# Kernel optimization log

Hardware: AMD Instinct MI355X
Metric: run time of the kernel (lower is better)

The kernel has to match this reference:

```python
import jax, jax.numpy as jnp
import numpy as np

ROPE_THETA = 10000.0

def apply_rope(x, positions):
    # x: [b, h, s, d], positions: [s]
    d = x.shape[-1]
    inv_freq = ROPE_THETA ** (-jnp.arange(0, d, 2, dtype=jnp.float32) / d)  # [d/2]
    ang = positions.astype(jnp.float32)[:, None] * inv_freq[None, :]        # [s, d/2]
    cos = jnp.cos(ang)
    sin = jnp.sin(ang)
    x1 = x[..., 0::2]
    x2 = x[..., 1::2]
    r1 = x1 * cos - x2 * sin
    r2 = x1 * sin + x2 * cos
    # interleave back to [..., d]
    return jnp.stack([r1, r2], axis=-1).reshape(x.shape)

def setup_inputs() -> dict:
    key = jax.random.key(0)
    k1, k2, k3 = jax.random.split(key, 3)
    b, s, d_model = 4, 2048, 1024
    x = jax.random.normal(k1, (b, s, d_model), dtype=jnp.float32)
    wqkv = jax.random.normal(k2, (3 * d_model, d_model), dtype=jnp.float32) * (d_model ** -0.5)
    wo = jax.random.normal(k3, (d_model, d_model), dtype=jnp.float32) * (d_model ** -0.5)
    token_positions = jnp.arange(s, dtype=jnp.int64 if jax.config.jax_enable_x64 else jnp.int32)
    return {"x": x, "wqkv": wqkv, "wo": wo, "token_positions": token_positions}

def reference(x, wqkv, wo, token_positions):
    b, s, d_model = x.shape
    num_heads = 16
    d_head = d_model // num_heads
    # fused QKV projection (Linear: y = x @ W.T)
    qkv = jnp.einsum('bse,fe->bsf', x, wqkv)  # [b, s, 3*d_model]
    q, k, v = jnp.split(qkv, 3, axis=-1)
    def to_heads(t):
        return t.reshape(b, s, num_heads, d_head).transpose(0, 2, 1, 3)  # [b, h, s, d]
    q, k, v = to_heads(q), to_heads(k), to_heads(v)
    q = apply_rope(q, token_positions)
    k = apply_rope(k, token_positions)
    scores = jnp.einsum('bhqd,bhkd->bhqk', q, k) / jnp.sqrt(jnp.asarray(d_head, dtype=x.dtype))
    causal = jnp.tril(jnp.ones((s, s), dtype=bool))  # [s, s]
    scores = jnp.where(causal, scores, -jnp.inf)
    weights = jax.nn.softmax(scores, axis=-1)
    y = jnp.einsum('bhqk,bhkd->bhqd', weights, v)
    y = y.transpose(0, 2, 1, 3).reshape(b, s, d_model)
    return jnp.einsum('bse,fe->bsf', y, wo)
```

## Files before the change

### kernel.cpp

```cpp
#include <hip/hip_runtime.h>
#include <stdint.h>


typedef __attribute__((ext_vector_type(8))) short bf16x8;
typedef __attribute__((ext_vector_type(4))) float f32x4;
typedef __attribute__((ext_vector_type(8))) unsigned short u16x8;
typedef __attribute__((ext_vector_type(4))) unsigned short u16x4;
typedef __attribute__((ext_vector_type(4))) unsigned int u32x4;

#define NB 4
#define NS 2048
#define NH 16
#define DH 64
#define DM 1024
#define BH (NB*NH)

static __device__ __forceinline__ unsigned short f2bf(float f){
  unsigned u = __builtin_bit_cast(unsigned, f);
  u += 0x7fffu + ((u >> 16) & 1u);
  return (unsigned short)(u >> 16);
}
static __device__ __forceinline__ float bf2f(unsigned short h){
  unsigned u = ((unsigned)h) << 16;
  return __builtin_bit_cast(float, u);
}
static __device__ __forceinline__ unsigned cvt_pk_bf16(float lo, float hi){
  unsigned r;
  asm("v_cvt_pk_bf16_f32 %0, %1, %2" : "=v"(r) : "v"(lo), "v"(hi));
  return r;
}
static __device__ __forceinline__ f32x4 mfma16(bf16x8 a, bf16x8 b, f32x4 c){
  return __builtin_amdgcn_mfma_f32_16x16x32_bf16(a, b, c, 0, 0, 0);
}
static __device__ __forceinline__ void gld_lds16(const void* g, void* l){
  __builtin_amdgcn_global_load_lds((const __attribute__((address_space(1))) unsigned int*)g,
                                   (__attribute__((address_space(3))) unsigned int*)l,
                                   16, 0, 0);
}

__global__ __launch_bounds__(256) void cvt_all(const float* __restrict__ x,
                                               const float* __restrict__ wqkv,
                                               const float* __restrict__ wo,
                                               const int* __restrict__ pos,
                                               unsigned short* __restrict__ xb,
                                               unsigned short* __restrict__ wqkvb,
                                               unsigned short* __restrict__ wob,
                                               float* __restrict__ ct,
                                               float* __restrict__ st){
  int stride = gridDim.x * blockDim.x;
  for (int i = blockIdx.x * blockDim.x + threadIdx.x; i < 3211264; i += stride){
    if (i < 3145728){
      const float* src; unsigned short* dst; int j;
      if (i < 2097152){ src = x; dst = xb; j = i; }
      else if (i < 2883584){ src = wqkv; dst = wqkvb; j = i - 2097152; }
      else { src = wo; dst = wob; j = i - 2883584; }
      f32x4 v = *(const f32x4*)(src + (size_t)j * 4);
      u16x4 o;
      o[0] = f2bf(v[0]); o[1] = f2bf(v[1]); o[2] = f2bf(v[2]); o[3] = f2bf(v[3]);
      *(u16x4*)(dst + (size_t)j * 4) = o;
    } else {
      int t = i - 3145728;
      int s = t >> 5, fi = t & 31;
      float p = (float)pos[s];
      float freq = exp2f(-(float)(2 * fi) * (13.287712379549449f / 64.f));
      float a = p * freq;
      ct[t] = cosf(a);
      st[t] = sinf(a);
    }
  }
}

__global__ __launch_bounds__(256) void rope_qk(unsigned short* __restrict__ buf,
                                               const float* __restrict__ ct,
                                               const float* __restrict__ st){
  size_t t  = (size_t)blockIdx.x * 256 + threadIdx.x;
  size_t e0 = t * 8;
  int dh0 = (int)(e0 & 63);
  int s   = (int)((e0 >> 6) & (NS - 1));
  u16x8 v = *(const u16x8*)(buf + e0);
  f32x4 c  = *(const f32x4*)(ct + s * 32 + (dh0 >> 1));
  f32x4 sn = *(const f32x4*)(st + s * 32 + (dh0 >> 1));
  u16x8 o;
#pragma unroll
  for (int i = 0; i < 4; i++){
    float x1 = bf2f(v[2*i]), x2 = bf2f(v[2*i+1]);
    o[2*i]   = f2bf(x1 * c[i] - x2 * sn[i]);
    o[2*i+1] = f2bf(x1 * sn[i] + x2 * c[i]);
  }
  *(u16x8*)(buf + e0) = o;
}

template<int BM, int BN, int MF, int NFR, int EPI, int RING, int OCC>
__global__ __launch_bounds__((BM/(MF*16))*(BN/(NFR*16))*64, OCC)
void gemm_ring(const unsigned short* __restrict__ A,
               const unsigned short* __restrict__ Bm,
               void* __restrict__ out0, void* __restrict__ out1,
               void* __restrict__ out2, int M, int N, int K){
  constexpr int WM = BM / (MF * 16);
  constexpr int WN = BN / (NFR * 16);
  constexpr int T  = WM * WN * 64;
  constexpr int LA = BM * 4 / T;
  constexpr int LB = BN * 4 / T;
  constexpr int L  = LA + LB;
  __shared__ __attribute__((aligned(16))) unsigned short As[RING][BM * 32];
  __shared__ __attribute__((aligned(16))) unsigned short Bs[RING][BN * 32];
  int tid = threadIdx.x;
  int w = tid >> 6, l = tid & 63;
  int lr = l & 15, lk = l >> 4;
  int m0 = blockIdx.y * BM, n0 = blockIdx.x * BN;
  int wr = (w / WN) * (MF * 16), wc = (w % WN) * (NFR * 16);

  const int nt = K >> 5;

  auto stage = [&](int t, int buf){
    int k0 = t * 32;
#pragma unroll
    for (int i = 0; i < LA; i++){
      int f = i * T + tid;
      int row = f >> 2, c = f & 3;
      int gc = (c ^ ((row >> 1) & 3)) * 8;
      gld_lds16(A + (size_t)(m0 + row) * K + k0 + gc, &As[buf][(i * T + w * 64) * 8]);
    }
#pragma unroll
    for (int i = 0; i < LB; i++){
      int f = i * T + tid;
      int row = f >> 2, c = f & 3;
      int gc = (c ^ ((row >> 1) & 3)) * 8;
      gld_lds16(Bm + (size_t)(n0 + row) * K + k0 + gc, &Bs[buf][(i * T + w * 64) * 8]);
    }
  };

  f32x4 zero = {0.f, 0.f, 0.f, 0.f};
  f32x4 acc[MF][NFR];
#pragma unroll
  for (int a = 0; a < MF; a++)
#pragma unroll
    for (int b = 0; b < NFR; b++) acc[a][b] = zero;

#pragma unroll
  for (int p = 0; p < RING - 1; p++) stage(p, p);
  asm volatile("s_waitcnt vmcnt(%0)" :: "i"((RING - 2) * L) : "memory");
  __builtin_amdgcn_sched_barrier(0);
  __builtin_amdgcn_s_barrier();
  __builtin_amdgcn_sched_barrier(0);

  int buf = 0;
  for (int t = 0; t < nt; ++t){
    bf16x8 af[MF], bfr[NFR];
#pragma unroll
    for (int mf = 0; mf < MF; mf++){
      int row = wr + mf * 16 + lr;
      af[mf] = *(const bf16x8*)&As[buf][row * 32 + ((lk ^ ((row >> 1) & 3)) * 8)];
    }
#pragma unroll
    for (int nf = 0; nf < NFR; nf++){
      int row = wc + nf * 16 + lr;
      bfr[nf] = *(const bf16x8*)&Bs[buf][row * 32 + ((lk ^ ((row >> 1) & 3)) * 8)];
    }
    if (t + RING - 1 < nt){
      int sb = buf - 1; if (sb < 0) sb = RING - 1;
      stage(t + RING - 1, sb);
    }
    __builtin_amdgcn_s_setprio(1);
#pragma unroll
    for (int mf = 0; mf < MF; mf++)
#pragma unroll
      for (int nf = 0; nf < NFR; nf++)
        acc[mf][nf] = mfma16(af[mf], bfr[nf], acc[mf][nf]);
    __builtin_amdgcn_s_setprio(0);
    if (RING >= 4){
      if (t + 3 < nt)      { asm volatile("s_waitcnt vmcnt(%0)" :: "i"(2 * L) : "memory"); }
      else if (t + 2 < nt) { asm volatile("s_waitcnt vmcnt(%0)" :: "i"(L) : "memory"); }
      else if (t + 1 < nt) { asm volatile("s_waitcnt vmcnt(0)" ::: "memory"); }
    } else {
      if (t + 2 < nt)      { asm volatile("s_waitcnt vmcnt(%0)" :: "i"(L) : "memory"); }
      else if (t + 1 < nt) { asm volatile("s_waitcnt vmcnt(0)" ::: "memory"); }
    }
    __builtin_amdgcn_sched_barrier(0);
    __builtin_amdgcn_s_barrier();
    __builtin_amdgcn_sched_barrier(0);
    buf = buf + 1; if (buf == RING) buf = 0;
  }

  if (EPI == 0){
    unsigned short* q  = (unsigned short*)out0;
    unsigned short* k  = (unsigned short*)out1;
    unsigned short* vt = (unsigned short*)out2;
#pragma unroll
    for (int mf = 0; mf < MF; mf++)
#pragma unroll
      for (int nf = 0; nf < NFR; nf++)
#pragma unroll
        for (int j = 0; j < 4; j++){
          int m = m0 + wr + mf * 16 + lk * 4 + j;
          int n = n0 + wc + nf * 16 + lr;
          int part = n >> 10, c = n & 1023;
          int h = c >> 6, dh = c & 63;
          int b = m >> 11, s = m & (NS - 1);
          unsigned short val = f2bf(acc[mf][nf][j]);
          if (part == 2){
            vt[((size_t)((b * NH + h) * DH + dh)) * NS + s] = val;
          } else {
            size_t off = ((size_t)(b * NH + h) * NS + s) * DH + dh;
            ((part == 0) ? q : k)[off] = val;
          }
        }
  } else {
    float* C = (float*)out0;
#pragma unroll
    for (int mf = 0; mf < MF; mf++)
#pragma unroll
      for (int nf = 0; nf < NFR; nf++)
#pragma unroll
        for (int j = 0; j < 4; j++){
          int m = m0 + wr + mf * 16 + lk * 4 + j;
          int n = n0 + wc + nf * 16 + lr;
          C[(size_t)m * N + n] = acc[mf][nf][j];
        }
  }
}

__global__ __launch_bounds__(256, 3) void fa_kernel(const unsigned short* __restrict__ qb_,
                                                    const unsigned short* __restrict__ kbuf,
                                                    const unsigned short* __restrict__ vtb,
                                                    unsigned short* __restrict__ yb,
                                                    const float* __restrict__ ct_,
                                                    const float* __restrict__ st_){
  __shared__ __attribute__((aligned(16))) unsigned short Kl[2][4096];
  __shared__ __attribute__((aligned(16))) unsigned short Vl[2][4096];
  __shared__ __attribute__((aligned(16))) unsigned short Pl[4][32 * 76];
  int tid = threadIdx.x;
  int w = tid >> 6, l = tid & 63;
  int lr = l & 15, lk = l >> 4;
  int qb = 15 - blockIdx.y;
  int bh = blockIdx.x;
  int b = bh >> 4, h = bh & 15;
  int qr0 = qb * 128 + w * 32;
  const unsigned short* Q  = qb_  + (size_t)bh * NS * DH;
  const unsigned short* Kp = kbuf + (size_t)bh * NS * DH;
  const unsigned short* VT = vtb  + (size_t)bh * DH * NS;
  unsigned short* Pw = &Pl[w][0];

  int r8  = l >> 3;
  int swc = ((l & 7) ^ (r8 & 7)) * 8;

  auto stage = [&](int buf, int t){
    int kbase = t * 64;
    if (w < 2){
#pragma unroll
      for (int ii = 0; ii < 4; ii++){
        int i = w * 4 + ii;
        gld_lds16(Kp + (size_t)(kbase + i * 8 + r8) * DH + swc, &Kl[buf][i * 512]);
      }
    } else {
#pragma unroll
      for (int ii = 0; ii < 4; ii++){
        int i = (w - 2) * 4 + ii;
        gld_lds16(VT + (size_t)(i * 8 + r8) * NS + kbase + swc, &Vl[buf][i * 512]);
      }
    }
  };

  const float SC = 0.18033688011112042f;
  bf16x8 qf[2][2];
#pragma unroll
  for (int mf = 0; mf < 2; mf++){
    int srow = qr0 + mf * 16 + lr;
    const unsigned short* qrow = Q + (size_t)srow * DH;
    const float* ctr = ct_ + srow * 32;
    const float* str = st_ + srow * 32;
#pragma unroll
    for (int ks = 0; ks < 2; ks++){
      u16x8 raw = *(const u16x8*)(qrow + ks * 32 + lk * 8);
      f32x4 cc = *(const f32x4*)(ctr + ks * 16 + lk * 4);
      f32x4 ss = *(const f32x4*)(str + ks * 16 + lk * 4);
      u32x4 wds;
#pragma unroll
      for (int p = 0; p < 4; p++){
        float c2 = cc[p] * SC, s2 = ss[p] * SC;
        float x1 = bf2f(raw[2*p]), x2 = bf2f(raw[2*p+1]);
        wds[p] = cvt_pk_bf16(x1 * c2 - x2 * s2, x1 * s2 + x2 * c2);
      }
      qf[mf][ks] = __builtin_bit_cast(bf16x8, wds);
    }
  }

  f32x4 zero = {0.f, 0.f, 0.f, 0.f};
  f32x4 O[2][4];
  float lsum[2];
#pragma unroll
  for (int mf = 0; mf < 2; mf++){
#pragma unroll
    for (int nf = 0; nf < 4; nf++) O[mf][nf] = zero;
    lsum[mf] = 0.f;
  }

  const int ntile = 2 * qb + 2;

  stage(0, 0);
  __syncthreads();

  int cur = 0;
  for (int t = 0; t < ntile; ++t){
    int kbase = t * 64;
    if (t + 1 < ntile) stage(cur ^ 1, t + 1);

    if (kbase <= qr0 + 31){
      bf16x8 kf[4][2];
#pragma unroll
      for (int nf = 0; nf < 4; nf++){
        int row = nf * 16 + lr;
        int ro = row * 64, sw = (row & 7) << 3;
#pragma unroll
        for (int ks = 0; ks < 2; ks++)
          kf[nf][ks] = *(const bf16x8*)&Kl[cur][ro + ((ks * 32 + lk * 8) ^ sw)];
      }
      bf16x8 vf[2][4];
#pragma unroll
      for (int nfd = 0; nfd < 4; nfd++){
        int row = nfd * 16 + lr;
        int ro = row * 64, sw = (row & 7) << 3;
#pragma unroll
        for (int ks = 0; ks < 2; ks++)
          vf[ks][nfd] = *(const bf16x8*)&Vl[cur][ro + ((ks * 32 + lk * 8) ^ sw)];
      }

      f32x4 sa[2][4];
#pragma unroll
      for (int mf = 0; mf < 2; mf++)
#pragma unroll
        for (int nf = 0; nf < 4; nf++) sa[mf][nf] = zero;
#pragma unroll
      for (int nf = 0; nf < 4; nf++)
#pragma unroll
        for (int mf = 0; mf < 2; mf++){
          sa[mf][nf] = mfma16(kf[nf][0], qf[mf][0], sa[mf][nf]);
          sa[mf][nf] = mfma16(kf[nf][1], qf[mf][1], sa[mf][nf]);
        }

      bool domask = (kbase + 63 > qr0);

#pragma unroll
      for (int mf = 0; mf < 2; mf++){
        int qg = qr0 + mf * 16 + lr;
        float ls = 0.f;
#pragma unroll
        for (int nf = 0; nf < 4; nf++){
          float p4[4];
#pragma unroll
          for (int j = 0; j < 4; j++){
            float xx = sa[mf][nf][j];
            if (domask){
              int kg = kbase + nf * 16 + lk * 4 + j;
              if (kg > qg) xx = -__builtin_inff();
            }
            float p = exp2f(xx);
            ls += p;
            p4[j] = p;
          }
          unsigned d0 = cvt_pk_bf16(p4[0], p4[1]);
          unsigned d1 = cvt_pk_bf16(p4[2], p4[3]);
          int base = (mf * 16 + lr) * 76 + nf * 16 + lk * 4;
          *(unsigned*)&Pw[base]     = d0;
          *(unsigned*)&Pw[base + 2] = d1;
        }
        lsum[mf] += ls;
      }

      bf16x8 pf[2][2];
#pragma unroll
      for (int mf = 0; mf < 2; mf++)
#pragma unroll
        for (int ks = 0; ks < 2; ks++)
          pf[mf][ks] = *(const bf16x8*)&Pw[(mf * 16 + lr) * 76 + ks * 32 + lk * 8];
#pragma unroll
      for (int ks = 0; ks < 2; ks++)
#pragma unroll
        for (int nfd = 0; nfd < 4; nfd++)
#pragma unroll
          for (int mf = 0; mf < 2; mf++)
            O[mf][nfd] = mfma16(pf[mf][ks], vf[ks][nfd], O[mf][nfd]);
    }

    __syncthreads();
    cur ^= 1;
  }

#pragma unroll
  for (int mf = 0; mf < 2; mf++){
    lsum[mf] += __shfl_xor(lsum[mf], 16);
    lsum[mf] += __shfl_xor(lsum[mf], 32);
  }
#pragma unroll
  for (int mf = 0; mf < 2; mf++)
#pragma unroll
    for (int j = 0; j < 4; j++){
      float s = __shfl(lsum[mf], lk * 4 + j);
      float inv = 1.0f / s;
      int srow = qr0 + mf * 16 + lk * 4 + j;
      unsigned short* yp = yb + ((size_t)(b * NS + srow)) * DM + h * DH;
#pragma unroll
      for (int nfd = 0; nfd < 4; nfd++)
        yp[nfd * 16 + lr] = f2bf(O[mf][nfd][j] * inv);
    }
}

extern "C" void kernel_launch(void* const* d_in, const int* in_sizes, int n_in,
                              void* d_out, int out_size, void* d_ws, size_t ws_size,
                              hipStream_t stream){
  const float* x    = (const float*)d_in[0];
  const float* wqkv = (const float*)d_in[1];
  const float* wo   = (const float*)d_in[2];
  const int*   pos  = (const int*)d_in[3];
  float* out = (float*)d_out;

  char* ws = (char*)d_ws;
  size_t off = 0;
  auto alloc = [&](size_t bytes) -> void* {
    void* p = ws + off;
    off += (bytes + 255) & ~(size_t)255;
    return p;
  };
  const size_t NE = (size_t)BH * NS * DH;
  unsigned short* xb    = (unsigned short*)alloc((size_t)8192 * 1024 * 2);
  unsigned short* wqkvb = (unsigned short*)alloc((size_t)3072 * 1024 * 2);
  unsigned short* wob   = (unsigned short*)alloc((size_t)1024 * 1024 * 2);
  unsigned short* q  = (unsigned short*)alloc(NE * 2);
  unsigned short* k  = (unsigned short*)alloc(NE * 2);
  unsigned short* vt = (unsigned short*)alloc(NE * 2);
  unsigned short* y  = (unsigned short*)alloc(NE * 2);
  float* ct = (float*)alloc((size_t)NS * 32 * 4);
  float* st = (float*)alloc((size_t)NS * 32 * 4);

  cvt_all<<<3072, 256, 0, stream>>>(x, wqkv, wo, pos, xb, wqkvb, wob, ct, st);
  gemm_ring<128, 128, 4, 4, 0, 3, 3><<<dim3(24, 64), 256, 0, stream>>>(
      xb, wqkvb, q, k, vt, 8192, 3072, 1024);
  rope_qk<<<4096, 256, 0, stream>>>(k, ct, st);
  fa_kernel<<<dim3(64, 16), 256, 0, stream>>>(q, k, vt, y, ct, st);
  gemm_ring<128, 128, 4, 4, 1, 4, 2><<<dim3(8, 64), 256, 0, stream>>>(
      y, wob, out, nullptr, nullptr, 8192, 1024, 1024);
}
```

Measured before the change: 214.6 us.

## Add 256x256 eight-wave ping-pong GEMM kernel for QKV projection

Replaces the templated 128x128 ring-buffered GEMM for the QKV projection with a dedicated 256x256 tile kernel that uses 8 waves and double-buffered LDS. The main loop is split into four sub-phases, with barriers interleaving direct global-to-LDS loads, LDS fragment reads and MFMA bursts under raised priority. The larger tile is meant to improve operand reuse, and the fine-grained schedule is meant to overlap memory with matrix math. In exchange it uses 128KB of LDS, issues many barriers per iteration, and launches only 384 blocks, which can leave the CUs unevenly loaded. The epilogue still writes one scalar at a time, scattered across q, k and transposed v.

```diff
diff --git a/kernel.cpp b/kernel.cpp
--- a/kernel.cpp
+++ b/kernel.cpp
@@ -90,6 +90,169 @@
   *(u16x8*)(buf + e0) = o;
 }
 
+__global__ __launch_bounds__(512, 2)
+void gemm1_8p(const unsigned short* __restrict__ A,
+              const unsigned short* __restrict__ Bm,
+              unsigned short* __restrict__ q,
+              unsigned short* __restrict__ k,
+              unsigned short* __restrict__ vt){
+  const int K = 1024, nt = 16;
+  __shared__ __attribute__((aligned(16))) unsigned short As[2][2 * 8192];
+  __shared__ __attribute__((aligned(16))) unsigned short Bs[2][2 * 8192];
+  int tid = threadIdx.x;
+  int w = tid >> 6, l = tid & 63;
+  int lr = l & 15, lk = l >> 4;
+  int m0 = blockIdx.y * 256, n0 = blockIdx.x * 256;
+  int r8 = l >> 3;
+  int swc = ((l & 7) ^ (r8 & 7)) * 8;
+  int wa = w >> 2;
+  int hb = (w & 3) >> 1;
+  int rbb = ((w & 3) & 1) * 64;
+
+  auto stageA = [&](int t, int h){
+#pragma unroll
+    for (int j = 0; j < 2; j++){
+      int i2 = w * 2 + j;
+      gld_lds16(A + (size_t)(m0 + h * 128 + i2 * 8 + r8) * K + t * 64 + swc,
+                &As[t & 1][h * 8192 + i2 * 8 * 64]);
+    }
+  };
+  auto stageB = [&](int t, int h){
+#pragma unroll
+    for (int j = 0; j < 2; j++){
+      int i2 = w * 2 + j;
+      gld_lds16(Bm + (size_t)(n0 + h * 128 + i2 * 8 + r8) * K + t * 64 + swc,
+                &Bs[t & 1][h * 8192 + i2 * 8 * 64]);
+    }
+  };
+
+  bf16x8 af[4][2];
+  bf16x8 bQ0[2][2], bQ1[2][2];
+
+  auto dsA = [&](int buf, int mfh){
+#pragma unroll
+    for (int m4 = 0; m4 < 4; m4++){
+      int r = (mfh * 4 + m4) * 16 + lr;
+#pragma unroll
+      for (int ks = 0; ks < 2; ks++)
+        af[m4][ks] = *(const bf16x8*)&As[buf][wa * 8192 + r * 64 + (((4 * ks + lk) ^ (lr & 7)) * 8)];
+    }
+  };
+  auto dsB = [&](int buf, int nfh, bf16x8 (&bb)[2][2]){
+#pragma unroll
+    for (int n2 = 0; n2 < 2; n2++){
+      int rb = rbb + (nfh * 2 + n2) * 16 + lr;
+#pragma unroll
+      for (int ks = 0; ks < 2; ks++)
+        bb[n2][ks] = *(const bf16x8*)&Bs[buf][hb * 8192 + rb * 64 + (((4 * ks + lk) ^ (lr & 7)) * 8)];
+    }
+  };
+
+  f32x4 zero = {0.f, 0.f, 0.f, 0.f};
+  f32x4 acc[8][4];
+#pragma unroll
+  for (int a = 0; a < 8; a++)
+#pragma unroll
+    for (int b = 0; b < 4; b++) acc[a][b] = zero;
+
+  auto MMA = [&](int mfh, int nfh, bf16x8 (&bb)[2][2]){
+    __builtin_amdgcn_s_setprio(1);
+#pragma unroll
+    for (int m4 = 0; m4 < 4; m4++)
+#pragma unroll
+      for (int n2 = 0; n2 < 2; n2++)
+#pragma unroll
+        for (int ks = 0; ks < 2; ks++)
+          acc[mfh * 4 + m4][nfh * 2 + n2] =
+              mfma16(af[m4][ks], bb[n2][ks], acc[mfh * 4 + m4][nfh * 2 + n2]);
+    __builtin_amdgcn_s_setprio(0);
+  };
+
+#define BAR()    __builtin_amdgcn_s_barrier()
+#define SCHED0() __builtin_amdgcn_sched_barrier(0)
+#define LGKM0()  do { asm volatile("s_waitcnt lgkmcnt(0)" ::: "memory"); SCHED0(); } while(0)
+
+  stageA(0, 0); stageA(0, 1); stageB(0, 0); stageB(0, 1);
+  stageA(1, 0); stageA(1, 1); stageB(1, 0); stageB(1, 1);
+  asm volatile("s_waitcnt vmcnt(8)" ::: "memory");
+  SCHED0(); BAR(); SCHED0();
+
+  for (int i = 0; i < 8; ++i){
+    int t0 = 2 * i, t1 = 2 * i + 1;
+    bool sA1 = (i >= 1);
+    bool s02 = (t0 + 2 < nt);
+    bool s12 = (t1 + 2 < nt);
+
+    dsA(0, 0); dsB(0, 0, bQ0);
+    if (sA1) stageA(t1, 0);
+    BAR(); LGKM0();
+    MMA(0, 0, bQ0);
+    BAR();
+    dsB(0, 1, bQ1);
+    if (sA1) stageA(t1, 1);
+    BAR(); LGKM0();
+    MMA(0, 1, bQ1);
+    BAR();
+    dsA(0, 1);
+    if (s02) stageB(t0 + 2, 0);
+    BAR(); LGKM0();
+    MMA(1, 1, bQ1);
+    BAR();
+    if (s02) stageB(t0 + 2, 1);
+    if (s02) { asm volatile("s_waitcnt vmcnt(4)" ::: "memory"); }
+    else     { asm volatile("s_waitcnt vmcnt(0)" ::: "memory"); }
+    SCHED0(); BAR(); SCHED0();
+    MMA(1, 0, bQ0);
+    BAR();
+
+    dsA(1, 0); dsB(1, 0, bQ0);
+    if (s02) stageA(t0 + 2, 0);
+    BAR(); LGKM0();
+    MMA(0, 0, bQ0);
+    BAR();
+    dsB(1, 1, bQ1);
+    if (s02) stageA(t0 + 2, 1);
+    BAR(); LGKM0();
+    MMA(0, 1, bQ1);
+    BAR();
+    dsA(1, 1);
+    if (s12) stageB(t1 + 2, 0);
+    BAR(); LGKM0();
+    MMA(1, 1, bQ1);
+    BAR();
+    if (s12) stageB(t1 + 2, 1);
+    if (s12) { asm volatile("s_waitcnt vmcnt(4)" ::: "memory"); }
+    else     { asm volatile("s_waitcnt vmcnt(0)" ::: "memory"); }
+    SCHED0(); BAR(); SCHED0();
+    MMA(1, 0, bQ0);
+    BAR();
+  }
+#undef BAR
+#undef SCHED0
+#undef LGKM0
+
+  int wr = wa * 128, wc = (w & 3) * 64;
+#pragma unroll
+  for (int mf = 0; mf < 8; mf++)
+#pragma unroll
+    for (int nf = 0; nf < 4; nf++)
+#pragma unroll
+      for (int j = 0; j < 4; j++){
+        int m = m0 + wr + mf * 16 + lk * 4 + j;
+        int n = n0 + wc + nf * 16 + lr;
+        int part = n >> 10, c = n & 1023;
+        int h = c >> 6, dh = c & 63;
+        int b = m >> 11, s = m & (NS - 1);
+        unsigned short val = f2bf(acc[mf][nf][j]);
+        if (part == 2){
+          vt[((size_t)((b * NH + h) * DH + dh)) * NS + s] = val;
+        } else {
+          size_t off = ((size_t)(b * NH + h) * NS + s) * DH + dh;
+          ((part == 0) ? q : k)[off] = val;
+        }
+      }
+}
+
 template<int BM, int BN, int MF, int NFR, int EPI, int RING, int OCC>
 __global__ __launch_bounds__((BM/(MF*16))*(BN/(NFR*16))*64, OCC)
 void gemm_ring(const unsigned short* __restrict__ A,
@@ -433,8 +596,7 @@
   float* st = (float*)alloc((size_t)NS * 32 * 4);
 
   cvt_all<<<3072, 256, 0, stream>>>(x, wqkv, wo, pos, xb, wqkvb, wob, ct, st);
-  gemm_ring<128, 128, 4, 4, 0, 3, 3><<<dim3(24, 64), 256, 0, stream>>>(
-      xb, wqkvb, q, k, vt, 8192, 3072, 1024);
+  gemm1_8p<<<dim3(12, 32), 512, 0, stream>>>(xb, wqkvb, q, k, vt);
   rope_qk<<<4096, 256, 0, stream>>>(k, ct, st);
   fa_kernel<<<dim3(64, 16), 256, 0, stream>>>(q, k, vt, y, ct, st);
   gemm_ring<128, 128, 4, 4, 1, 4, 2><<<dim3(8, 64), 256, 0, stream>>>(
```

New measurement: 221.1 us. 3.0% more time.
